# Optimization experiments

Measured on AMD Instinct MI355X. Metric: run time of the kernel, lower is better.

The kernel has to match this reference:

```python
import jax, jax.numpy as jnp
import numpy as np

B, S, D, H = 2, 2048, 1024, 16
HD = D // H

def setup_inputs() -> dict:
    key = jax.random.key(0)
    ks = jax.random.split(key, 11)
    s = 1.0 / np.sqrt(D)
    return {
        "query": jax.random.normal(ks[0], (B, S, D), jnp.float32),
        "key": jax.random.normal(ks[1], (B, S, D), jnp.float32),
        "value": jax.random.normal(ks[2], (B, S, D), jnp.float32),
        "Wq": jax.random.normal(ks[3], (D, D), jnp.float32) * s,
        "bq": jax.random.normal(ks[4], (D,), jnp.float32) * s,
        "Wk": jax.random.normal(ks[5], (D, D), jnp.float32) * s,
        "bk": jax.random.normal(ks[6], (D,), jnp.float32) * s,
        "Wv": jax.random.normal(ks[7], (D, D), jnp.float32) * s,
        "bv": jax.random.normal(ks[8], (D,), jnp.float32) * s,
        "Wo": jax.random.normal(ks[9], (D, D), jnp.float32) * s,
        "bo": jax.random.normal(ks[10], (D,), jnp.float32) * s,
        "test": 0,
    }

def _heads(x, W, b):
    # [B,S,D] @ [D,D] -> [B,S,D] -> [B,H,S,HD]
    y = x @ W + b
    return y.reshape(B, -1, H, HD).transpose(0, 2, 1, 3)

def reference(query, key, value, Wq, bq, Wk, bk, Wv, bv, Wo, bo, test):
    q = _heads(query, Wq, bq)
    k = _heads(key, Wk, bk)
    v = _heads(value, Wv, bv)
    scale = 1.0 / np.sqrt(HD).astype(np.float32)
    scores = jnp.einsum('bhqd,bhkd->bhqk', q, k) * scale  # [B,H,S,S]
    if test:
        return scores
    prob = jax.nn.softmax(scores, axis=-1)
    out = jnp.einsum('bhqk,bhkd->bhqd', prob, v)
    out = out.transpose(0, 2, 1, 3).reshape(B, -1, D)
    return out @ Wo + bo
```

## Files before the change

### kernel.cpp

```cpp
#include <hip/hip_runtime.h>

constexpr int Bn  = 2;
constexpr int Sn  = 2048;
constexpr int Dn  = 1024;
constexpr int Hn  = 16;
constexpr int HDn = 64;
constexpr int Mn  = Bn * Sn;

typedef _Float16 half8 __attribute__((ext_vector_type(8)));
typedef _Float16 half4 __attribute__((ext_vector_type(4)));
typedef float    f32x4 __attribute__((ext_vector_type(4)));

__device__ __forceinline__ void cp16(const _Float16* g, _Float16* l) {
  __builtin_amdgcn_global_load_lds(
      (__attribute__((address_space(1))) void*)g,
      (__attribute__((address_space(3))) void*)l, 16, 0, 0);
}

__global__ __launch_bounds__(256) void convert_x(
    const float* __restrict__ q, const float* __restrict__ k,
    const float* __restrict__ v, _Float16* __restrict__ Xh) {
  const int z = blockIdx.y;
  const float* src = (z == 0) ? q : (z == 1) ? k : v;
  _Float16* dst = Xh + (size_t)z * (Mn * Dn);
  int i = blockIdx.x * 256 + threadIdx.x;
  float4 v4 = ((const float4*)src)[i];
  half4 h;
  h.x = (_Float16)v4.x; h.y = (_Float16)v4.y;
  h.z = (_Float16)v4.z; h.w = (_Float16)v4.w;
  *(half4*)(dst + (size_t)i * 4) = h;
}

__global__ __launch_bounds__(256) void transpose_w(
    const float* __restrict__ Wq, const float* __restrict__ Wk,
    const float* __restrict__ Wv, const float* __restrict__ Wo,
    _Float16* __restrict__ WT) {
  const int z = blockIdx.z;
  const float* W = (z == 0) ? Wq : (z == 1) ? Wk : (z == 2) ? Wv : Wo;
  _Float16* T = WT + (size_t)z * Dn * Dn;
  __shared__ float tile[64][65];
  const int k0 = blockIdx.y * 64, n0 = blockIdx.x * 64;
  const int tid = threadIdx.x;
#pragma unroll
  for (int i = 0; i < 4; i++) {
    int s = tid + i * 256;
    int r = s >> 4, c4 = s & 15;
    float4 w4 = *(const float4*)(W + (size_t)(k0 + r) * Dn + n0 + c4 * 4);
    tile[r][c4 * 4 + 0] = w4.x; tile[r][c4 * 4 + 1] = w4.y;
    tile[r][c4 * 4 + 2] = w4.z; tile[r][c4 * 4 + 3] = w4.w;
  }
  __syncthreads();
#pragma unroll
  for (int i = 0; i < 2; i++) {
    int s = tid + i * 256;
    int n = s >> 3, r8 = (s & 7) * 8;
    half8 h;
#pragma unroll
    for (int j = 0; j < 8; j++) h[j] = (_Float16)tile[r8 + j][n];
    *(half8*)(T + (size_t)(n0 + n) * Dn + k0 + r8) = h;
  }
}

__global__ __launch_bounds__(256) void proj_kernel(
    const _Float16* __restrict__ Xh, const _Float16* __restrict__ WT,
    const float* __restrict__ bq, const float* __restrict__ bk,
    const float* __restrict__ bv,
    _Float16* __restrict__ Qh, _Float16* __restrict__ Kh,
    _Float16* __restrict__ VT) {
  const int z = blockIdx.z;
  const _Float16* A  = Xh + (size_t)z * Mn * Dn;
  const _Float16* Bm = WT + (size_t)z * Dn * Dn;
  const float* bias = (z == 0) ? bq : (z == 1) ? bk : bv;

  __shared__ __align__(16) _Float16 As[128 * 32];
  __shared__ __align__(16) _Float16 Bs[128 * 32];

  const int tid  = threadIdx.x;
  const int lane = tid & 63;
  const int w    = tid >> 6;
  const int wm   = (w >> 1) * 64;
  const int wn   = (w & 1) * 64;
  const int m0   = blockIdx.y * 128;
  const int n0   = blockIdx.x * 128;
  const int qd   = lane >> 4;
  const int lm   = lane & 15;

  f32x4 acc[4][4];
#pragma unroll
  for (int i = 0; i < 4; i++)
#pragma unroll
    for (int j = 0; j < 4; j++) acc[i][j] = {0.f, 0.f, 0.f, 0.f};

  for (int k0 = 0; k0 < Dn; k0 += 32) {
#pragma unroll
    for (int p = 0; p < 2; p++) {
      int s = tid + p * 256;
      int row = s >> 2, c = s & 3;
      cp16(A + (size_t)(m0 + row) * Dn + k0 + c * 8, As + s * 8);
    }
#pragma unroll
    for (int p = 0; p < 2; p++) {
      int s = tid + p * 256;
      int row = s >> 2, c = s & 3;
      cp16(Bm + (size_t)(n0 + row) * Dn + k0 + c * 8, Bs + s * 8);
    }
    __syncthreads();
    half8 a[4], bb[4];
#pragma unroll
    for (int mi = 0; mi < 4; mi++)
      a[mi] = *(const half8*)(As + (wm + mi * 16 + lm) * 32 + qd * 8);
#pragma unroll
    for (int ni = 0; ni < 4; ni++)
      bb[ni] = *(const half8*)(Bs + (wn + ni * 16 + lm) * 32 + qd * 8);
    if (z < 2) {
#pragma unroll
      for (int mi = 0; mi < 4; mi++)
#pragma unroll
        for (int ni = 0; ni < 4; ni++)
          acc[mi][ni] = __builtin_amdgcn_mfma_f32_16x16x32_f16(bb[ni], a[mi], acc[mi][ni], 0, 0, 0);
    } else {
#pragma unroll
      for (int mi = 0; mi < 4; mi++)
#pragma unroll
        for (int ni = 0; ni < 4; ni++)
          acc[mi][ni] = __builtin_amdgcn_mfma_f32_16x16x32_f16(a[mi], bb[ni], acc[mi][ni], 0, 0, 0);
    }
    __syncthreads();
  }

  if (z < 2) {
    _Float16* out = (z == 0) ? Qh : Kh;
    const float scl = (z == 0) ? 0.125f * 1.44269504089f : 1.0f;
#pragma unroll
    for (int mi = 0; mi < 4; mi++) {
      int m = m0 + wm + mi * 16 + lm;
      int b_ = m >> 11, s_ = m & (Sn - 1);
#pragma unroll
      for (int ni = 0; ni < 4; ni++) {
        int nb = n0 + wn + ni * 16 + qd * 4;
        float4 b4 = *(const float4*)(bias + nb);
        int h = nb >> 6, hd = nb & 63;
        half4 h4;
        h4[0] = (_Float16)((acc[mi][ni][0] + b4.x) * scl);
        h4[1] = (_Float16)((acc[mi][ni][1] + b4.y) * scl);
        h4[2] = (_Float16)((acc[mi][ni][2] + b4.z) * scl);
        h4[3] = (_Float16)((acc[mi][ni][3] + b4.w) * scl);
        *(half4*)(out + (((size_t)(b_ * Hn + h)) * Sn + s_) * HDn + hd) = h4;
      }
    }
  } else {
#pragma unroll
    for (int ni = 0; ni < 4; ni++) {
      int n = n0 + wn + ni * 16 + lm;
      float b_f = bias[n];
      int h = n >> 6, hd = n & 63;
#pragma unroll
      for (int mi = 0; mi < 4; mi++) {
        int mb = m0 + wm + mi * 16 + qd * 4;
        int b_ = mb >> 11, s_ = mb & (Sn - 1);
        half4 h4;
#pragma unroll
        for (int r = 0; r < 4; r++) h4[r] = (_Float16)(acc[mi][ni][r] + b_f);
        *(half4*)(VT + (((size_t)(b_ * Hn + h)) * HDn + hd) * Sn + s_) = h4;
      }
    }
  }
}

__global__ __launch_bounds__(256) void attn_kernel(
    const _Float16* __restrict__ Qh, const _Float16* __restrict__ Kh,
    const _Float16* __restrict__ VT, _Float16* __restrict__ attn_out) {
  constexpr int PV_LD = 136;
  __shared__ __align__(16) _Float16 Ksb[2][128 * 64];
  __shared__ __align__(16) _Float16 Ps[4 * 32 * PV_LD];

  const int bh = blockIdx.y;
  const int q0 = blockIdx.x * 128;
  const size_t base = (size_t)bh * Sn * HDn;

  const int tid  = threadIdx.x;
  const int lane = tid & 63;
  const int w    = tid >> 6;
  const int qd   = lane >> 4;
  const int lm   = lane & 15;

  const _Float16* qptr = Qh + base + (size_t)(q0 + w * 32 + lm) * HDn + qd * 8;
  half8 qa[2][2];
#pragma unroll
  for (int nj = 0; nj < 2; nj++)
#pragma unroll
    for (int ks = 0; ks < 2; ks++)
      qa[nj][ks] = *(const half8*)(qptr + nj * 16 * HDn + ks * 32);

  half8 vones;
#pragma unroll
  for (int j = 0; j < 8; j++) vones[j] = (lm == 0) ? (_Float16)1.0f : (_Float16)0.0f;

  f32x4 oacc[2][4];
#pragma unroll
  for (int i = 0; i < 2; i++)
#pragma unroll
    for (int j = 0; j < 4; j++) oacc[i][j] = {0.f, 0.f, 0.f, 0.f};
  f32x4 oaccl[2] = {{0.f, 0.f, 0.f, 0.f}, {0.f, 0.f, 0.f, 0.f}};

  _Float16* Psw = Ps + w * (32 * PV_LD);
  const f32x4 sinit = {-10.f, -10.f, -10.f, -10.f};

  const int st_r  = tid >> 3;
  const int st_u  = (tid & 7) ^ (st_r & 7);
  const _Float16* kbase = Kh + base;

#define STAGE_K(KT, DST)                                                     \
  {                                                                          \
    const _Float16* src_ = kbase + (size_t)(KT) * 128 * HDn;                 \
    _Float16* dst_ = (DST);                                                  \
    _Pragma("unroll")                                                        \
    for (int p = 0; p < 4; p++)                                              \
      cp16(src_ + (size_t)(st_r + p * 32) * HDn + st_u * 8,                  \
           dst_ + (tid + p * 256) * 8);                                      \
  }

  STAGE_K(0, Ksb[0])
  __syncthreads();

  int cur = 0;
  for (int kt = 0; kt < Sn / 128; kt++) {
    const int kb = kt * 128;
    if (kt + 1 < Sn / 128) STAGE_K(kt + 1, Ksb[cur ^ 1])

    f32x4 sacc[8][2];
#pragma unroll
    for (int ni = 0; ni < 8; ni++)
#pragma unroll
      for (int nj = 0; nj < 2; nj++) sacc[ni][nj] = sinit;
#pragma unroll
    for (int ni = 0; ni < 8; ni++)
#pragma unroll
      for (int ks = 0; ks < 2; ks++) {
        int up = (4 * ks + qd) ^ (lm & 7);
        half8 ka = *(const half8*)(Ksb[cur] + (ni * 16 + lm) * HDn + up * 8);
#pragma unroll
        for (int nj = 0; nj < 2; nj++)
          sacc[ni][nj] = __builtin_amdgcn_mfma_f32_16x16x32_f16(ka, qa[nj][ks], sacc[ni][nj], 0, 0, 0);
      }

    half8 vb[4][4];
#pragma unroll
    for (int oi = 0; oi < 4; oi++)
#pragma unroll
      for (int ks = 0; ks < 4; ks++)
        vb[oi][ks] = *(const half8*)(VT + base + (size_t)(oi * 16 + lm) * Sn + kb + ks * 32 + qd * 8);

#pragma unroll
    for (int nj = 0; nj < 2; nj++)
#pragma unroll
      for (int ni = 0; ni < 8; ni++) {
        float p0 = __builtin_amdgcn_exp2f(sacc[ni][nj][0]);
        float p1 = __builtin_amdgcn_exp2f(sacc[ni][nj][1]);
        float p2 = __builtin_amdgcn_exp2f(sacc[ni][nj][2]);
        float p3 = __builtin_amdgcn_exp2f(sacc[ni][nj][3]);
        auto lo = __builtin_amdgcn_cvt_pkrtz(p0, p1);
        auto hi = __builtin_amdgcn_cvt_pkrtz(p2, p3);
        half4 h4;
        h4[0] = (_Float16)lo[0]; h4[1] = (_Float16)lo[1];
        h4[2] = (_Float16)hi[0]; h4[3] = (_Float16)hi[1];
        *(half4*)(Psw + (nj * 16 + lm) * PV_LD + ni * 16 + qd * 4) = h4;
      }

#pragma unroll
    for (int ks = 0; ks < 4; ks++) {
      half8 pa[2];
#pragma unroll
      for (int mi = 0; mi < 2; mi++)
        pa[mi] = *(const half8*)(Psw + (mi * 16 + lm) * PV_LD + ks * 32 + qd * 8);
#pragma unroll
      for (int oi = 0; oi < 4; oi++)
#pragma unroll
        for (int mi = 0; mi < 2; mi++)
          oacc[mi][oi] = __builtin_amdgcn_mfma_f32_16x16x32_f16(vb[oi][ks], pa[mi], oacc[mi][oi], 0, 0, 0);
#pragma unroll
      for (int mi = 0; mi < 2; mi++)
        oaccl[mi] = __builtin_amdgcn_mfma_f32_16x16x32_f16(vones, pa[mi], oaccl[mi], 0, 0, 0);
    }

    __syncthreads();
    cur ^= 1;
  }
#undef STAGE_K

  const int b_ = bh >> 4, h_ = bh & 15;
#pragma unroll
  for (int mi = 0; mi < 2; mi++) {
    float lr = __shfl(oaccl[mi][0], lm, 64);
    float inv = 1.0f / lr;
    int qrow = q0 + w * 32 + mi * 16 + lm;
    size_t rowbase = ((size_t)(b_ * Sn + qrow)) * Dn + h_ * 64;
#pragma unroll
    for (int oi = 0; oi < 4; oi++) {
      half4 h4;
#pragma unroll
      for (int r = 0; r < 4; r++) h4[r] = (_Float16)(oacc[mi][oi][r] * inv);
      *(half4*)(attn_out + rowbase + oi * 16 + qd * 4) = h4;
    }
  }
}

__global__ __launch_bounds__(256) void outproj_kernel(
    const _Float16* __restrict__ Aattn, const _Float16* __restrict__ WoT,
    const float* __restrict__ bo, float* __restrict__ out) {
  __shared__ __align__(16) _Float16 As[128 * 32];
  __shared__ __align__(16) _Float16 Bs[128 * 32];

  const int tid  = threadIdx.x;
  const int lane = tid & 63;
  const int w    = tid >> 6;
  const int wm   = (w >> 1) * 64;
  const int wn   = (w & 1) * 64;
  const int m0   = blockIdx.y * 128;
  const int n0   = blockIdx.x * 128;
  const int qd   = lane >> 4;
  const int lm   = lane & 15;

  f32x4 acc[4][4];
#pragma unroll
  for (int i = 0; i < 4; i++)
#pragma unroll
    for (int j = 0; j < 4; j++) acc[i][j] = {0.f, 0.f, 0.f, 0.f};

  for (int k0 = 0; k0 < Dn; k0 += 32) {
#pragma unroll
    for (int p = 0; p < 2; p++) {
      int s = tid + p * 256;
      int row = s >> 2, c = s & 3;
      cp16(Aattn + (size_t)(m0 + row) * Dn + k0 + c * 8, As + s * 8);
    }
#pragma unroll
    for (int p = 0; p < 2; p++) {
      int s = tid + p * 256;
      int row = s >> 2, c = s & 3;
      cp16(WoT + (size_t)(n0 + row) * Dn + k0 + c * 8, Bs + s * 8);
    }
    __syncthreads();
    half8 a[4], bb[4];
#pragma unroll
    for (int mi = 0; mi < 4; mi++)
      a[mi] = *(const half8*)(As + (wm + mi * 16 + lm) * 32 + qd * 8);
#pragma unroll
    for (int ni = 0; ni < 4; ni++)
      bb[ni] = *(const half8*)(Bs + (wn + ni * 16 + lm) * 32 + qd * 8);
#pragma unroll
    for (int mi = 0; mi < 4; mi++)
#pragma unroll
      for (int ni = 0; ni < 4; ni++)
        acc[mi][ni] = __builtin_amdgcn_mfma_f32_16x16x32_f16(bb[ni], a[mi], acc[mi][ni], 0, 0, 0);
    __syncthreads();
  }
#pragma unroll
  for (int mi = 0; mi < 4; mi++) {
    int m = m0 + wm + mi * 16 + lm;
#pragma unroll
    for (int ni = 0; ni < 4; ni++) {
      int nb = n0 + wn + ni * 16 + qd * 4;
      float4 b4 = *(const float4*)(bo + nb);
      float4 o4;
      o4.x = acc[mi][ni][0] + b4.x;
      o4.y = acc[mi][ni][1] + b4.y;
      o4.z = acc[mi][ni][2] + b4.z;
      o4.w = acc[mi][ni][3] + b4.w;
      *(float4*)(out + (size_t)m * Dn + nb) = o4;
    }
  }
}

extern "C" void kernel_launch(void* const* d_in, const int* in_sizes, int n_in,
                              void* d_out, int out_size, void* d_ws, size_t ws_size,
                              hipStream_t stream) {
  const float* query = (const float*)d_in[0];
  const float* key_  = (const float*)d_in[1];
  const float* value = (const float*)d_in[2];
  const float* Wq = (const float*)d_in[3];
  const float* bq = (const float*)d_in[4];
  const float* Wk = (const float*)d_in[5];
  const float* bk = (const float*)d_in[6];
  const float* Wv = (const float*)d_in[7];
  const float* bv = (const float*)d_in[8];
  const float* Wo = (const float*)d_in[9];
  const float* bo = (const float*)d_in[10];

  _Float16* Xh = (_Float16*)d_ws;
  _Float16* WT = Xh + (size_t)3 * Mn * Dn;
  _Float16* Qh = WT + (size_t)4 * Dn * Dn;
  _Float16* Kh = Qh + (size_t)Mn * Dn;
  _Float16* VT = Kh + (size_t)Mn * Dn;
  _Float16* attnb = Xh;
  float* out = (float*)d_out;

  dim3 blk(256);
  convert_x<<<dim3((Mn * Dn) / (4 * 256), 3), blk, 0, stream>>>(query, key_, value, Xh);
  transpose_w<<<dim3(16, 16, 4), blk, 0, stream>>>(Wq, Wk, Wv, Wo, WT);
  proj_kernel<<<dim3(Dn / 128, Mn / 128, 3), blk, 0, stream>>>(
      Xh, WT, bq, bk, bv, Qh, Kh, VT);
  attn_kernel<<<dim3(Sn / 128, Bn * Hn), blk, 0, stream>>>(Qh, Kh, VT, attnb);
  outproj_kernel<<<dim3(Dn / 128, Mn / 128), blk, 0, stream>>>(
      attnb, WT + (size_t)3 * Dn * Dn, bo, out);
}
```

Measured before the change: 275.8 us.

## Split attention KV tile into halves to cut registers and remap blocks

The attention inner loop now processes each 128-key tile as two 64-key chunks. Score accumulators, V fragments and the P staging buffer are halved, and launch bounds request 3 blocks per SM to raise occupancy. The grid is flattened to 1D and remapped so consecutive blocks spread across heads and batches, which changes L2 locality and XCD distribution. The trade-off is more LDS write/read round trips per tile and possible register spills if the bound is too tight.

```diff
diff --git a/kernel.cpp b/kernel.cpp
--- a/kernel.cpp
+++ b/kernel.cpp
@@ -167,15 +167,17 @@
   }
 }
 
-__global__ __launch_bounds__(256) void attn_kernel(
+__global__ __launch_bounds__(256, 3) void attn_kernel(
     const _Float16* __restrict__ Qh, const _Float16* __restrict__ Kh,
     const _Float16* __restrict__ VT, _Float16* __restrict__ attn_out) {
-  constexpr int PV_LD = 136;
+  constexpr int PV_LD = 72;
   __shared__ __align__(16) _Float16 Ksb[2][128 * 64];
   __shared__ __align__(16) _Float16 Ps[4 * 32 * PV_LD];
 
-  const int bh = blockIdx.y;
-  const int q0 = blockIdx.x * 128;
+  const int n    = blockIdx.x;
+  const int slot = n >> 3;
+  const int bh   = (n & 7) * 4 + (slot >> 4);
+  const int q0   = (slot & 15) * 128;
   const size_t base = (size_t)bh * Sn * HDn;
 
   const int tid  = threadIdx.x;
@@ -206,8 +208,8 @@
   _Float16* Psw = Ps + w * (32 * PV_LD);
   const f32x4 sinit = {-10.f, -10.f, -10.f, -10.f};
 
-  const int st_r  = tid >> 3;
-  const int st_u  = (tid & 7) ^ (st_r & 7);
+  const int st_r = tid >> 3;
+  const int st_u = (tid & 7) ^ (st_r & 7);
   const _Float16* kbase = Kh + base;
 
 #define STAGE_K(KT, DST)                                                     \
@@ -228,59 +230,65 @@
     const int kb = kt * 128;
     if (kt + 1 < Sn / 128) STAGE_K(kt + 1, Ksb[cur ^ 1])
 
-    f32x4 sacc[8][2];
-#pragma unroll
-    for (int ni = 0; ni < 8; ni++)
-#pragma unroll
-      for (int nj = 0; nj < 2; nj++) sacc[ni][nj] = sinit;
-#pragma unroll
-    for (int ni = 0; ni < 8; ni++)
-#pragma unroll
-      for (int ks = 0; ks < 2; ks++) {
-        int up = (4 * ks + qd) ^ (lm & 7);
-        half8 ka = *(const half8*)(Ksb[cur] + (ni * 16 + lm) * HDn + up * 8);
-#pragma unroll
-        for (int nj = 0; nj < 2; nj++)
-          sacc[ni][nj] = __builtin_amdgcn_mfma_f32_16x16x32_f16(ka, qa[nj][ks], sacc[ni][nj], 0, 0, 0);
+#pragma unroll
+    for (int c = 0; c < 2; c++) {
+      f32x4 sacc[4][2];
+#pragma unroll
+      for (int n4 = 0; n4 < 4; n4++)
+#pragma unroll
+        for (int nj = 0; nj < 2; nj++) sacc[n4][nj] = sinit;
+#pragma unroll
+      for (int n4 = 0; n4 < 4; n4++) {
+        int ni = 4 * c + n4;
+#pragma unroll
+        for (int ks = 0; ks < 2; ks++) {
+          int up = (4 * ks + qd) ^ (lm & 7);
+          half8 ka = *(const half8*)(Ksb[cur] + (ni * 16 + lm) * HDn + up * 8);
+#pragma unroll
+          for (int nj = 0; nj < 2; nj++)
+            sacc[n4][nj] = __builtin_amdgcn_mfma_f32_16x16x32_f16(ka, qa[nj][ks], sacc[n4][nj], 0, 0, 0);
+        }
       }
 
-    half8 vb[4][4];
-#pragma unroll
-    for (int oi = 0; oi < 4; oi++)
-#pragma unroll
-      for (int ks = 0; ks < 4; ks++)
-        vb[oi][ks] = *(const half8*)(VT + base + (size_t)(oi * 16 + lm) * Sn + kb + ks * 32 + qd * 8);
-
-#pragma unroll
-    for (int nj = 0; nj < 2; nj++)
-#pragma unroll
-      for (int ni = 0; ni < 8; ni++) {
-        float p0 = __builtin_amdgcn_exp2f(sacc[ni][nj][0]);
-        float p1 = __builtin_amdgcn_exp2f(sacc[ni][nj][1]);
-        float p2 = __builtin_amdgcn_exp2f(sacc[ni][nj][2]);
-        float p3 = __builtin_amdgcn_exp2f(sacc[ni][nj][3]);
-        auto lo = __builtin_amdgcn_cvt_pkrtz(p0, p1);
-        auto hi = __builtin_amdgcn_cvt_pkrtz(p2, p3);
-        half4 h4;
-        h4[0] = (_Float16)lo[0]; h4[1] = (_Float16)lo[1];
-        h4[2] = (_Float16)hi[0]; h4[3] = (_Float16)hi[1];
-        *(half4*)(Psw + (nj * 16 + lm) * PV_LD + ni * 16 + qd * 4) = h4;
+      half8 vb[4][2];
+#pragma unroll
+      for (int oi = 0; oi < 4; oi++)
+#pragma unroll
+        for (int k2 = 0; k2 < 2; k2++)
+          vb[oi][k2] = *(const half8*)(VT + base + (size_t)(oi * 16 + lm) * Sn
+                                       + kb + c * 64 + k2 * 32 + qd * 8);
+
+#pragma unroll
+      for (int nj = 0; nj < 2; nj++)
+#pragma unroll
+        for (int n4 = 0; n4 < 4; n4++) {
+          float p0 = __builtin_amdgcn_exp2f(sacc[n4][nj][0]);
+          float p1 = __builtin_amdgcn_exp2f(sacc[n4][nj][1]);
+          float p2 = __builtin_amdgcn_exp2f(sacc[n4][nj][2]);
+          float p3 = __builtin_amdgcn_exp2f(sacc[n4][nj][3]);
+          auto lo = __builtin_amdgcn_cvt_pkrtz(p0, p1);
+          auto hi = __builtin_amdgcn_cvt_pkrtz(p2, p3);
+          half4 h4;
+          h4[0] = (_Float16)lo[0]; h4[1] = (_Float16)lo[1];
+          h4[2] = (_Float16)hi[0]; h4[3] = (_Float16)hi[1];
+          *(half4*)(Psw + (nj * 16 + lm) * PV_LD + n4 * 16 + qd * 4) = h4;
+        }
+
+#pragma unroll
+      for (int k2 = 0; k2 < 2; k2++) {
+        half8 pa[2];
+#pragma unroll
+        for (int mi = 0; mi < 2; mi++)
+          pa[mi] = *(const half8*)(Psw + (mi * 16 + lm) * PV_LD + k2 * 32 + qd * 8);
+#pragma unroll
+        for (int oi = 0; oi < 4; oi++)
+#pragma unroll
+          for (int mi = 0; mi < 2; mi++)
+            oacc[mi][oi] = __builtin_amdgcn_mfma_f32_16x16x32_f16(vb[oi][k2], pa[mi], oacc[mi][oi], 0, 0, 0);
+#pragma unroll
+        for (int mi = 0; mi < 2; mi++)
+          oaccl[mi] = __builtin_amdgcn_mfma_f32_16x16x32_f16(vones, pa[mi], oaccl[mi], 0, 0, 0);
       }
-
-#pragma unroll
-    for (int ks = 0; ks < 4; ks++) {
-      half8 pa[2];
-#pragma unroll
-      for (int mi = 0; mi < 2; mi++)
-        pa[mi] = *(const half8*)(Psw + (mi * 16 + lm) * PV_LD + ks * 32 + qd * 8);
-#pragma unroll
-      for (int oi = 0; oi < 4; oi++)
-#pragma unroll
-        for (int mi = 0; mi < 2; mi++)
-          oacc[mi][oi] = __builtin_amdgcn_mfma_f32_16x16x32_f16(vb[oi][ks], pa[mi], oacc[mi][oi], 0, 0, 0);
-#pragma unroll
-      for (int mi = 0; mi < 2; mi++)
-        oaccl[mi] = __builtin_amdgcn_mfma_f32_16x16x32_f16(vones, pa[mi], oaccl[mi], 0, 0, 0);
     }
 
     __syncthreads();
@@ -400,7 +408,7 @@
   transpose_w<<<dim3(16, 16, 4), blk, 0, stream>>>(Wq, Wk, Wv, Wo, WT);
   proj_kernel<<<dim3(Dn / 128, Mn / 128, 3), blk, 0, stream>>>(
       Xh, WT, bq, bk, bv, Qh, Kh, VT);
-  attn_kernel<<<dim3(Sn / 128, Bn * Hn), blk, 0, stream>>>(Qh, Kh, VT, attnb);
+  attn_kernel<<<dim3(512), blk, 0, stream>>>(Qh, Kh, VT, attnb);
   outproj_kernel<<<dim3(Dn / 128, Mn / 128), blk, 0, stream>>>(
       attnb, WT + (size_t)3 * Dn * Dn, bo, out);
 }
```

Result: no change. 274.6 us (-0.4%).
